# Kernel tuning notes

Hardware: AMD Instinct MI355X
Metric: run time of the kernel (lower is better)

The kernel has to match this reference:

```python
import jax, jax.numpy as jnp
import numpy as np
from jax import lax

NUM_TAGS = 19
IN_DIM = 202
HID = 100
B, T = 256, 512


def setup_inputs() -> dict:
    key = jax.random.key(0)
    ks = jax.random.split(key, 16)
    u = lambda k, shape, s: jax.random.uniform(k, shape, jnp.float32, -s, s)
    sh = 1.0 / np.sqrt(HID)
    sl = 1.0 / np.sqrt(2 * HID)
    x = jax.random.normal(ks[0], (B, T, IN_DIM), jnp.float32)
    lengths = jax.random.randint(ks[1], (B,), 1, T + 1)
    raw_tags = jax.random.randint(ks[2], (B, T), 0, NUM_TAGS)
    y = jnp.where(jnp.arange(T)[None, :] < lengths[:, None], raw_tags, -1)
    return dict(
        x=x, y=y,
        w_ih_f=u(ks[3], (HID, IN_DIM), sh), w_hh_f=u(ks[4], (HID, HID), sh),
        b_ih_f=u(ks[5], (HID,), sh), b_hh_f=u(ks[6], (HID,), sh),
        w_ih_b=u(ks[7], (HID, IN_DIM), sh), w_hh_b=u(ks[8], (HID, HID), sh),
        b_ih_b=u(ks[9], (HID,), sh), b_hh_b=u(ks[10], (HID,), sh),
        w_lin=u(ks[11], (NUM_TAGS, 2 * HID), sl), b_lin=u(ks[12], (NUM_TAGS,), sl),
        start_trans=u(ks[13], (NUM_TAGS,), 0.1),
        end_trans=u(ks[14], (NUM_TAGS,), 0.1),
        trans=u(ks[15], (NUM_TAGS, NUM_TAGS), 0.1),
    )


def _rnn_dir(x, w_ih, w_hh, b_ih, b_hh, reverse):
    # torch nn.RNN (tanh) scans over axis 0 of x (batch_first=False semantics)
    def step(h, xt):
        h = jnp.tanh(xt @ w_ih.T + b_ih + h @ w_hh.T + b_hh)
        return h, h
    h0 = jnp.zeros((x.shape[1], w_hh.shape[0]), x.dtype)
    _, hs = lax.scan(step, h0, x, reverse=reverse)
    return hs  # (S, N, HID)


def _emissions(x, w_ih_f, w_hh_f, b_ih_f, b_hh_f, w_ih_b, w_hh_b, b_ih_b, b_hh_b, w_lin, b_lin):
    hf = _rnn_dir(x, w_ih_f, w_hh_f, b_ih_f, b_hh_f, False)
    hb = _rnn_dir(x, w_ih_b, w_hh_b, b_ih_b, b_hh_b, True)
    h = jnp.concatenate([hf, hb], axis=-1)  # (B, T, 200)
    return jax.nn.softmax(h @ w_lin.T + b_lin, axis=2)  # (B, T, 19)


def _crf_llh(em, tags, mask, start, end, trans):
    # emissions (B,T,K) batch_first -> transpose to (T,B,*) for the scans
    em_t = jnp.swapaxes(em, 0, 1)
    tg = jnp.where(jnp.swapaxes(mask, 0, 1), jnp.swapaxes(tags, 0, 1), 0)
    mk = jnp.swapaxes(mask, 0, 1)
    mf = mk.astype(em.dtype)
    # numerator: gold path score
    s0 = start[tg[0]] + jnp.take_along_axis(em_t[0], tg[0][:, None], 1)[:, 0]
    def num_step(carry, inp):
        s, prev = carry
        e, t, m, mb = inp
        emit = jnp.take_along_axis(e, t[:, None], 1)[:, 0]
        s = s + (trans[prev, t] + emit) * m
        prev = jnp.where(mb, t, prev)  # track tag at last valid position
        return (s, prev), None
    (num, last), _ = lax.scan(num_step, (s0, tg[0]), (em_t[1:], tg[1:], mf[1:], mk[1:]))
    num = num + end[last]
    # denominator: masked forward algorithm
    def z_step(s, inp):
        e, mb = inp
        nxt = jax.nn.logsumexp(s[:, :, None] + trans[None] + e[:, None, :], axis=1)
        return jnp.where(mb[:, None], nxt, s), None
    z, _ = lax.scan(z_step, start + em_t[0], (em_t[1:], mk[1:]))
    logz = jax.nn.logsumexp(z + end, axis=1)
    return num - logz  # (B,) log-likelihood per sequence


def _viterbi(em, mask, start, end, trans):
    em_t = jnp.swapaxes(em, 0, 1)
    mk = jnp.swapaxes(mask, 0, 1)
    def fstep(s, inp):
        e, mb = inp
        cand = s[:, :, None] + trans[None] + e[:, None, :]  # (B,K,K)
        nxt = jnp.where(mb[:, None], jnp.max(cand, axis=1), s)
        return nxt, jnp.argmax(cand, axis=1)
    score, hist = lax.scan(fstep, start + em_t[0], (em_t[1:], mk[1:]))  # hist (T-1,B,K)
    best_last = jnp.argmax(score + end, axis=1)  # tag at each sequence end
    def bstep(tag, inp):
        h, mb = inp
        prev = jnp.take_along_axis(h, tag[:, None], 1)[:, 0]
        tag = jnp.where(mb, prev, tag)
        return tag, tag
    _, tags_bt = lax.scan(bstep, best_last, (hist, mk[1:]), reverse=True)  # (T-1,B), position order
    tags = jnp.concatenate([tags_bt, best_last[None]], axis=0)  # (T,B)
    tags = jnp.swapaxes(tags, 0, 1)
    return jnp.where(mask, tags, -1)  # pad with -1 like the torch pad_sequence


def reference(x, y, w_ih_f, w_hh_f, b_ih_f, b_hh_f, w_ih_b, w_hh_b, b_ih_b, b_hh_b, w_lin, b_lin, start_trans, end_trans, trans):
    mask = y != -1
    em = _emissions(x, w_ih_f, w_hh_f, b_ih_f, b_hh_f, w_ih_b, w_hh_b, b_ih_b, b_hh_b, w_lin, b_lin)
    loss = -jnp.sum(_crf_llh(em, y, mask, start_trans, end_trans, trans))  # reduction='sum'
    label = _viterbi(em, mask, start_trans, end_trans, trans)
    return loss, label
```

## Files before the change

### kernel.cpp

```cpp
#include <hip/hip_runtime.h>
#include <hip/hip_bf16.h>

#define B_ 256
#define T_ 512
#define IN_ 202
#define HID_ 100
#define K_ 19

typedef __attribute__((ext_vector_type(8))) short short8v;
typedef __attribute__((ext_vector_type(4))) float f32x4;

__device__ __forceinline__ float rl_f(float v, int l) {
  return __int_as_float(__builtin_amdgcn_readlane(__float_as_int(v), l));
}
__device__ __forceinline__ float bcast_f(float v, int l) {
  return __int_as_float(__builtin_amdgcn_ds_bpermute(l * 4, __float_as_int(v)));
}
__device__ __forceinline__ float fast_tanh(float x) {
  float t = __expf(2.f * x);
  float r = __builtin_amdgcn_rcpf(t + 1.f);
  return fmaf(-2.f, r, 1.f);
}

__global__ __launch_bounds__(256, 1) void k_wprep(
    const float* __restrict__ wf, const float* __restrict__ wb,
    unsigned short* __restrict__ w3) {
  int idx = blockIdx.x * 256 + threadIdx.x;
  if (idx >= 224 * 224) return;
  int c = idx / 224, k = idx - (idx / 224) * 224;
  float v = 0.f;
  if (k < IN_) {
    if (c < 100) v = wf[c * IN_ + k];
    else if (c < 200) v = wb[(c - 100) * IN_ + k];
  }
  unsigned u0 = __float_as_uint(v) & 0xffff0000u;
  float r1 = v - __uint_as_float(u0);
  unsigned u1 = __float_as_uint(r1) & 0xffff0000u;
  float r2 = r1 - __uint_as_float(u1);
  w3[idx] = (unsigned short)(u0 >> 16);
  w3[50176 + idx] = (unsigned short)(u1 >> 16);
  w3[100352 + idx] = (unsigned short)(__float_as_uint(r2) >> 16);
}

__global__ __launch_bounds__(256, 2) void k_ih(
    const float* __restrict__ x, const unsigned short* __restrict__ w3,
    const float* __restrict__ bif, const float* __restrict__ bhf,
    const float* __restrict__ bib, const float* __restrict__ bhb,
    float* __restrict__ pre) {
  __shared__ float xs[128 * 36];
  __shared__ float bsum[224];
  int tid = threadIdx.x;
  int wv = tid >> 6, l = tid & 63;
  long row0 = (long)blockIdx.x * 128;
  for (int u = tid; u < 224; u += 256) {
    float bv = 0.f;
    if (u < 100) bv = bif[u] + bhf[u];
    else if (u < 200) bv = bib[u - 100] + bhb[u - 100];
    bsum[u] = bv;
  }
  int lr = l & 15;
  int kq = l >> 4;
  f32x4 acc[2][14];
#pragma unroll
  for (int m = 0; m < 2; m++)
#pragma unroll
    for (int n = 0; n < 14; n++) acc[m][n] = (f32x4){0.f, 0.f, 0.f, 0.f};
  for (int ck = 0; ck < 7; ck++) {
    int k0 = ck * 32;
    __syncthreads();
#pragma unroll
    for (int i = 0; i < 8; i++) {
      int u = tid + i * 256;
      int r = u >> 4, kp = u & 15;
      int gk = k0 + 2 * kp;
      float2 v = make_float2(0.f, 0.f);
      if (gk < IN_) v = *(const float2*)(x + (row0 + r) * IN_ + gk);
      *(float2*)(&xs[r * 36 + 2 * kp]) = v;
    }
    __syncthreads();
    short8v A0[2], A1[2], A2[2];
#pragma unroll
    for (int m = 0; m < 2; m++) {
      const float* ap = &xs[(wv * 32 + m * 16 + lr) * 36 + kq * 8];
      float4 fa = *(const float4*)(ap);
      float4 fb = *(const float4*)(ap + 4);
      float f[8] = {fa.x, fa.y, fa.z, fa.w, fb.x, fb.y, fb.z, fb.w};
#pragma unroll
      for (int j = 0; j < 8; j++) {
        unsigned u0 = __float_as_uint(f[j]) & 0xffff0000u;
        float r1 = f[j] - __uint_as_float(u0);
        unsigned u1 = __float_as_uint(r1) & 0xffff0000u;
        float r2 = r1 - __uint_as_float(u1);
        A0[m][j] = (short)(u0 >> 16);
        A1[m][j] = (short)(u1 >> 16);
        A2[m][j] = (short)(__float_as_uint(r2) >> 16);
      }
    }
#pragma unroll
    for (int n = 0; n < 14; n++) {
      int col = n * 16 + lr;
      const unsigned short* bp = w3 + (long)col * 224 + k0 + kq * 8;
      short8v B0 = *(const short8v*)(bp);
      short8v B1 = *(const short8v*)(bp + 50176);
      short8v B2 = *(const short8v*)(bp + 100352);
#pragma unroll
      for (int m = 0; m < 2; m++) {
        f32x4 c = acc[m][n];
        c = __builtin_amdgcn_mfma_f32_16x16x32_bf16(A0[m], B0, c, 0, 0, 0);
        c = __builtin_amdgcn_mfma_f32_16x16x32_bf16(A0[m], B1, c, 0, 0, 0);
        c = __builtin_amdgcn_mfma_f32_16x16x32_bf16(A1[m], B0, c, 0, 0, 0);
        c = __builtin_amdgcn_mfma_f32_16x16x32_bf16(A0[m], B2, c, 0, 0, 0);
        c = __builtin_amdgcn_mfma_f32_16x16x32_bf16(A2[m], B0, c, 0, 0, 0);
        c = __builtin_amdgcn_mfma_f32_16x16x32_bf16(A1[m], B1, c, 0, 0, 0);
        c = __builtin_amdgcn_mfma_f32_16x16x32_bf16(A1[m], B2, c, 0, 0, 0);
        c = __builtin_amdgcn_mfma_f32_16x16x32_bf16(A2[m], B1, c, 0, 0, 0);
        acc[m][n] = c;
      }
    }
  }
#pragma unroll
  for (int m = 0; m < 2; m++) {
    long rbase = row0 + wv * 32 + m * 16 + kq * 4;
#pragma unroll
    for (int n = 0; n < 13; n++) {
      int col = n * 16 + lr;
      if (col < 200) {
        float bv = bsum[col];
#pragma unroll
        for (int r = 0; r < 4; r++)
          pre[(rbase + r) * 200 + col] = acc[m][n][r] + bv;
      }
    }
  }
}

template <int KO, int KN, bool OW>
__device__ __forceinline__ void rnn8(
    float* __restrict__ p, long step, int row, bool owns, int qidx,
    const float* __restrict__ w, float (*hb)[104], float (*ps)[104]) {
  float wr[KN];
#pragma unroll
  for (int i = 0; i < KN / 4; i++) {
    float4 w4 = *(const float4*)(w + row * HID_ + KO + 4 * i);
    wr[4 * i + 0] = w4.x; wr[4 * i + 1] = w4.y;
    wr[4 * i + 2] = w4.z; wr[4 * i + 3] = w4.w;
  }
  float a = 0.f;
  if (OW) a = p[row];
  for (int s = 0; s < B_; s++) {
    int cur = s & 1;
    float a_next = 0.f;
    if (OW && s < B_ - 1) a_next = p[step + row];
    float ac0 = OW ? a : 0.f, ac1 = 0.f, ac2 = 0.f, ac3 = 0.f;
#pragma unroll
    for (int i = 0; i < KN / 4; i++) {
      float4 h4 = *(const float4*)(&hb[cur][KO + 4 * i]);
      ac0 = fmaf(h4.x, wr[4 * i + 0], ac0);
      ac1 = fmaf(h4.y, wr[4 * i + 1], ac1);
      ac2 = fmaf(h4.z, wr[4 * i + 2], ac2);
      ac3 = fmaf(h4.w, wr[4 * i + 3], ac3);
    }
    float partial = (ac0 + ac1) + (ac2 + ac3);
    if (!OW && owns) ps[qidx][row] = partial;
    __syncthreads();
    if (OW) {
      float tot = partial + ps[0][row] + ps[1][row] + ps[2][row];
      float hnew = fast_tanh(tot);
      if (owns) {
        p[row] = hnew;
        hb[cur ^ 1][row] = hnew;
      }
    }
    __syncthreads();
    p += step;
    a = a_next;
  }
}

__global__ __launch_bounds__(512, 8) void k_rnn(
    float* __restrict__ pre,
    const float* __restrict__ whf, const float* __restrict__ whb) {
  __shared__ __align__(16) float hb[2][104];
  __shared__ __align__(16) float ps[3][104];
  int bid = blockIdx.x;
  int dir = bid >> 9;
  int t = bid & 511;
  const float* w = dir ? whb : whf;
  int tid = threadIdx.x;
  int wv = tid >> 6, lane = tid & 63;
  int grp = wv & 1;
  int kq = wv >> 1;
  int row = grp ? (64 + (lane < 36 ? lane : 35)) : lane;
  bool owns = grp ? (lane < 36) : true;
  long step = dir ? -(long)(T_ * 200) : (long)(T_ * 200);
  float* p = pre + ((long)(dir ? (B_ - 1) : 0) * T_ + t) * 200 + dir * 100;
  if (tid < 104) hb[0][tid] = 0.f;
  __syncthreads();
  if (kq == 0)      rnn8<0, 16, true >(p, step, row, owns, 0, w, hb, ps);
  else if (kq == 1) rnn8<16, 28, false>(p, step, row, owns, 0, w, hb, ps);
  else if (kq == 2) rnn8<44, 28, false>(p, step, row, owns, 1, w, hb, ps);
  else              rnn8<72, 28, false>(p, step, row, owns, 2, w, hb, ps);
}

__global__ __launch_bounds__(256, 4) void k_lin(
    const float* __restrict__ h, const float* __restrict__ wlin,
    const float* __restrict__ blin, float* __restrict__ em) {
  int tid = threadIdx.x;
  long r0 = ((long)blockIdx.x * 256 + tid) * 2;
  const float* h0 = h + r0 * 200;
  float acc0[K_], acc1[K_];
#pragma unroll
  for (int c = 0; c < K_; c++) { float bb = blin[c]; acc0[c] = bb; acc1[c] = bb; }
  for (int kk = 0; kk < 50; kk++) {
    float4 a = *(const float4*)(h0 + 4 * kk);
    float4 b = *(const float4*)(h0 + 200 + 4 * kk);
#pragma unroll
    for (int c = 0; c < K_; c++) {
      float4 wv = *(const float4*)(wlin + c * 200 + 4 * kk);
      acc0[c] += a.x * wv.x + a.y * wv.y + a.z * wv.z + a.w * wv.w;
      acc1[c] += b.x * wv.x + b.y * wv.y + b.z * wv.z + b.w * wv.w;
    }
  }
  float mx0 = acc0[0], mx1 = acc1[0];
#pragma unroll
  for (int c = 1; c < K_; c++) { mx0 = fmaxf(mx0, acc0[c]); mx1 = fmaxf(mx1, acc1[c]); }
  float s0 = 0.f, s1 = 0.f;
#pragma unroll
  for (int c = 0; c < K_; c++) {
    acc0[c] = __expf(acc0[c] - mx0); s0 += acc0[c];
    acc1[c] = __expf(acc1[c] - mx1); s1 += acc1[c];
  }
  float i0 = 1.f / s0, i1 = 1.f / s1;
  float* e0 = em + r0 * K_;
#pragma unroll
  for (int c = 0; c < K_; c++) { e0[c] = acc0[c] * i0; e0[K_ + c] = acc1[c] * i1; }
}

__global__ __launch_bounds__(128, 1) void k_crf(
    const float* __restrict__ em, const int* __restrict__ y,
    const float* __restrict__ st_g, const float* __restrict__ en_g,
    const float* __restrict__ tr_g,
    float* __restrict__ part, int* __restrict__ cnt,
    float* __restrict__ out) {
  __shared__ __align__(16) float es[T_ * K_];
  __shared__ int ys[T_];
  __shared__ float trs[K_ * K_];
  __shared__ float st[K_], en[K_];
  __shared__ unsigned char hl[511 * K_ + 13];
  int b = blockIdx.x;
  int tid = threadIdx.x;
  int wv = tid >> 6, lane = tid & 63;
  const float4* eb4 = (const float4*)(em + (long)b * T_ * K_);
  for (int u = tid; u < T_ * K_ / 4; u += 128) ((float4*)es)[u] = eb4[u];
  for (int u = tid; u < T_; u += 128) ys[u] = y[b * T_ + u];
  for (int u = tid; u < K_ * K_; u += 128) trs[u] = tr_g[u];
  if (tid < K_) { st[tid] = st_g[tid]; en[tid] = en_g[tid]; }
  __syncthreads();
  int lmin = T_;
  for (int u = lane; u < T_; u += 64)
    if (ys[u] == -1 && u < lmin) lmin = u;
#pragma unroll
  for (int off = 32; off; off >>= 1) {
    int o = __shfl_xor(lmin, off, 64);
    lmin = lmin < o ? lmin : o;
  }
  int len = lmin;

  int jj = lane < K_ ? lane : K_ - 1;
  bool act = lane < K_;
  float enr[20];
#pragma unroll
  for (int q = 0; q < 5; q++) {
    float4 e4 = (q < 4) ? *(const float4*)(&en[4 * q])
                        : make_float4(en[16], en[17], en[18], -1e30f);
    enr[4 * q] = e4.x; enr[4 * q + 1] = e4.y; enr[4 * q + 2] = e4.z; enr[4 * q + 3] = e4.w;
  }

  if (wv == 0) {
    float gacc = 0.f;
    for (int t = 1 + lane; t < len; t += 64)
      gacc += trs[ys[t - 1] * K_ + ys[t]] + es[t * K_ + ys[t]];
#pragma unroll
    for (int off = 32; off; off >>= 1) gacc += __shfl_xor(gacc, off, 64);
    int y0 = ys[0], ylast = ys[len - 1];
    float num = st[y0] + es[y0] + gacc + en[ylast];
    float Ecol[K_];
#pragma unroll
    for (int i = 0; i < K_; i++) Ecol[i] = __expf(trs[i * K_ + jj]);
    float P = __expf(st[jj] + es[jj]);
    int kacc = 0;
    float ee = __expf(es[K_ + jj]);
    for (int t = 1; t < len; t++) {
      float pr[K_];
#pragma unroll
      for (int i = 0; i < K_; i++) pr[i] = bcast_f(P, i);
      int tn = (t + 1 < T_) ? t + 1 : T_ - 1;
      float e_next = es[tn * K_ + jj];
      unsigned pb = __float_as_uint(pr[0]);
      int ex = (int)((pb >> 23) & 0xff);
      float scale = __uint_as_float((unsigned)(254 - ex) << 23);
      kacc += ex - 127;
      float a0 = 0.f, a1 = 0.f, a2 = 0.f, a3 = 0.f;
#pragma unroll
      for (int i = 0; i < K_; i++) {
        if ((i & 3) == 0)      a0 = fmaf(pr[i], Ecol[i], a0);
        else if ((i & 3) == 1) a1 = fmaf(pr[i], Ecol[i], a1);
        else if ((i & 3) == 2) a2 = fmaf(pr[i], Ecol[i], a2);
        else                   a3 = fmaf(pr[i], Ecol[i], a3);
      }
      P = (((a0 + a1) + (a2 + a3)) * ee) * scale;
      ee = __expf(e_next);
    }
    {
      float pr[K_];
#pragma unroll
      for (int i = 0; i < K_; i++) pr[i] = bcast_f(P, i);
      float sm = 0.f;
#pragma unroll
      for (int i = 0; i < K_; i++) sm += pr[i] * __expf(enr[i]);
      if (lane == 0) part[b] = __logf(sm) + (float)kacc * 0.6931471805599453f - num;
    }
    int old = -1;
    if (lane == 0) { __threadfence(); old = atomicAdd(cnt, 1); }
    old = __shfl(old, 0, 64);
    if (old == B_ - 1) {
      __threadfence();
      float s = 0.f;
      for (int u = lane; u < B_; u += 64) s += part[u];
#pragma unroll
      for (int off = 32; off; off >>= 1) s += __shfl_xor(s, off, 64);
      if (lane == 0) out[0] = s;
    }
  } else {
    float Tt[K_];
#pragma unroll
    for (int i = 0; i < K_; i++) Tt[i] = trs[i * K_ + jj];
    float V = st[jj] + es[jj];
    float e = es[K_ + jj];
    for (int t = 1; t < len; t++) {
      float vr[K_];
#pragma unroll
      for (int i = 0; i < K_; i++) vr[i] = bcast_f(V, i);
      int tn = (t + 1 < T_) ? t + 1 : T_ - 1;
      float e_next = es[tn * K_ + jj];
      float b0 = -1e30f, b1 = -1e30f, b2 = -1e30f, b3 = -1e30f;
      int a0 = 0, a1 = 5, a2 = 10, a3 = 15;
#pragma unroll
      for (int i = 0; i < 5; i++)  { float c = vr[i] + Tt[i]; if (c > b0) { b0 = c; a0 = i; } }
#pragma unroll
      for (int i = 5; i < 10; i++) { float c = vr[i] + Tt[i]; if (c > b1) { b1 = c; a1 = i; } }
#pragma unroll
      for (int i = 10; i < 15; i++){ float c = vr[i] + Tt[i]; if (c > b2) { b2 = c; a2 = i; } }
#pragma unroll
      for (int i = 15; i < 19; i++){ float c = vr[i] + Tt[i]; if (c > b3) { b3 = c; a3 = i; } }
      if (b1 > b0) { b0 = b1; a0 = a1; }
      if (b2 > b0) { b0 = b2; a0 = a2; }
      if (b3 > b0) { b0 = b3; a0 = a3; }
      if (act) hl[(t - 1) * K_ + lane] = (unsigned char)a0;
      V = b0 + e;
      e = e_next;
    }
    int aa;
    {
      float vr[K_];
#pragma unroll
      for (int i = 0; i < K_; i++) vr[i] = bcast_f(V, i);
      float bb = vr[0] + enr[0]; aa = 0;
#pragma unroll
      for (int i = 1; i < K_; i++) {
        float c = vr[i] + enr[i];
        if (c > bb) { bb = c; aa = i; }
      }
    }
    float* ob = out + 1 + (long)b * T_;
    for (int u = lane; u < T_; u += 64)
      if (u >= len) ob[u] = -1.f;
    int tag = aa;
    if (lane == 0) ob[len - 1] = (float)tag;
    int vc = (act && len >= 2) ? (int)hl[(len - 2) * K_ + lane] : 0;
    for (int ti = len - 2; ti >= 0; ti--) {
      int vn = 0;
      if (ti > 0 && act) vn = (int)hl[(ti - 1) * K_ + lane];
      int ts = __builtin_amdgcn_readfirstlane(tag);
      tag = __builtin_amdgcn_readlane(vc, ts);
      if (lane == 0) ob[ti] = (float)tag;
      vc = vn;
    }
  }
}

extern "C" void kernel_launch(void* const* d_in, const int* in_sizes, int n_in,
                              void* d_out, int out_size, void* d_ws, size_t ws_size,
                              hipStream_t stream) {
  const float* x      = (const float*)d_in[0];
  const int*   y      = (const int*)d_in[1];
  const float* w_ih_f = (const float*)d_in[2];
  const float* w_hh_f = (const float*)d_in[3];
  const float* b_ih_f = (const float*)d_in[4];
  const float* b_hh_f = (const float*)d_in[5];
  const float* w_ih_b = (const float*)d_in[6];
  const float* w_hh_b = (const float*)d_in[7];
  const float* b_ih_b = (const float*)d_in[8];
  const float* b_hh_b = (const float*)d_in[9];
  const float* w_lin  = (const float*)d_in[10];
  const float* b_lin  = (const float*)d_in[11];
  const float* st     = (const float*)d_in[12];
  const float* en     = (const float*)d_in[13];
  const float* trans  = (const float*)d_in[14];

  char* ws = (char*)d_ws;
  const size_t PRE_OFF  = 0;
  const size_t EM_OFF   = 104857600;
  const size_t PART_OFF = EM_OFF + 9961472;
  const size_t CNT_OFF  = PART_OFF + 1024;
  float* PRE  = (float*)(ws + PRE_OFF);
  float* EM   = (float*)(ws + EM_OFF);
  float* PART = (float*)(ws + PART_OFF);
  int*   CNT  = (int*)(ws + CNT_OFF);
  unsigned short* W3 = (unsigned short*)(ws + EM_OFF);
  float* out  = (float*)d_out;

  hipMemsetAsync((void*)CNT, 0, sizeof(int), stream);
  k_wprep<<<196, 256, 0, stream>>>(w_ih_f, w_ih_b, W3);
  k_ih<<<1024, 256, 0, stream>>>(x, W3, b_ih_f, b_hh_f, b_ih_b, b_hh_b, PRE);
  k_rnn<<<1024, 512, 0, stream>>>(PRE, w_hh_f, w_hh_b);
  k_lin<<<256, 256, 0, stream>>>(PRE, w_lin, b_lin, EM);
  k_crf<<<256, 128, 0, stream>>>(EM, y, st, en, trans, PART, CNT, out);
}
```

Before: 578.5 us.

## Parallelize CRF forward and Viterbi scans via chunked semiring matrix products

Replaces the serial per-timestep CRF forward-algorithm and Viterbi recurrences with a chunked scan. The 512-step sequence is split into 16-step chunks whose max-plus and sum-product transfer matrices are built in parallel by many wavefronts. Short serial passes then combine the chunk matrices, and Viterbi backpointers are recomputed per chunk from the stored boundary scores. This shortens the serial dependency chain at the cost of far more total arithmetic, 512 threads per block and a large dynamic LDS allocation. The linear-domain chunk products could also lose precision, since rescaling happens only at chunk boundaries.

Measured after the change: 1.431 ms. +147.4%, slower.

```diff
diff --git a/kernel.cpp b/kernel.cpp
--- a/kernel.cpp
+++ b/kernel.cpp
@@ -6,6 +6,25 @@
 #define IN_ 202
 #define HID_ 100
 #define K_ 19
+#define NCH 32
+#define CL 16
+#define MSTRIDE 368
+
+#define MV_OFF   0
+#define MP_OFF   (MV_OFF + NCH * MSTRIDE)
+#define TRT_OFF  (MP_OFF + NCH * MSTRIDE)
+#define ETL_OFF  (TRT_OFF + 380)
+#define BV_OFF   (ETL_OFF + 380)
+#define VF_OFF   (BV_OFF + 640)
+#define PF_OFF   (VF_OFF + 20)
+#define STL_OFF  (PF_OFF + 20)
+#define ENL_OFF  (STL_OFF + 20)
+#define NUM_OFF  (ENL_OFF + 20)
+#define KC_OFF   (NUM_OFF + 2)
+#define FLT_END  (KC_OFF + 2)
+#define HL_OFF_B 100544
+#define LEN_OFF_B (HL_OFF_B + 9728)
+#define CRF_LDS_B (LEN_OFF_B + 64)
 
 typedef __attribute__((ext_vector_type(8))) short short8v;
 typedef __attribute__((ext_vector_type(4))) float f32x4;
@@ -236,147 +255,260 @@
   for (int c = 0; c < K_; c++) { e0[c] = acc0[c] * i0; e0[K_ + c] = acc1[c] * i1; }
 }
 
-__global__ __launch_bounds__(128, 1) void k_crf(
+__global__ __launch_bounds__(512, 1) void k_crf(
     const float* __restrict__ em, const int* __restrict__ y,
     const float* __restrict__ st_g, const float* __restrict__ en_g,
     const float* __restrict__ tr_g,
     float* __restrict__ part, int* __restrict__ cnt,
     float* __restrict__ out) {
-  __shared__ __align__(16) float es[T_ * K_];
-  __shared__ int ys[T_];
-  __shared__ float trs[K_ * K_];
-  __shared__ float st[K_], en[K_];
-  __shared__ unsigned char hl[511 * K_ + 13];
+  extern __shared__ __align__(16) float S[];
+  unsigned char* hl = (unsigned char*)S + HL_OFF_B;
+  int* lenp = (int*)((char*)S + LEN_OFF_B);
   int b = blockIdx.x;
   int tid = threadIdx.x;
   int wv = tid >> 6, lane = tid & 63;
-  const float4* eb4 = (const float4*)(em + (long)b * T_ * K_);
-  for (int u = tid; u < T_ * K_ / 4; u += 128) ((float4*)es)[u] = eb4[u];
-  for (int u = tid; u < T_; u += 128) ys[u] = y[b * T_ + u];
-  for (int u = tid; u < K_ * K_; u += 128) trs[u] = tr_g[u];
-  if (tid < K_) { st[tid] = st_g[tid]; en[tid] = en_g[tid]; }
-  __syncthreads();
-  int lmin = T_;
-  for (int u = lane; u < T_; u += 64)
-    if (ys[u] == -1 && u < lmin) lmin = u;
-#pragma unroll
-  for (int off = 32; off; off >>= 1) {
-    int o = __shfl_xor(lmin, off, 64);
-    lmin = lmin < o ? lmin : o;
-  }
-  int len = lmin;
-
-  int jj = lane < K_ ? lane : K_ - 1;
-  bool act = lane < K_;
-  float enr[20];
-#pragma unroll
-  for (int q = 0; q < 5; q++) {
-    float4 e4 = (q < 4) ? *(const float4*)(&en[4 * q])
-                        : make_float4(en[16], en[17], en[18], -1e30f);
-    enr[4 * q] = e4.x; enr[4 * q + 1] = e4.y; enr[4 * q + 2] = e4.z; enr[4 * q + 3] = e4.w;
-  }
-
+  const float* eb = em + (long)b * T_ * K_;
+  const int* yb = y + (long)b * T_;
+  if (tid < 380) {
+    int j = tid / 20, k = tid - (tid / 20) * 20;
+    float tv = (k < 19) ? tr_g[k * 19 + j] : 0.f;
+    S[TRT_OFF + tid] = tv;
+    S[ETL_OFF + tid] = (k < 19) ? __expf(tv) : 0.f;
+  }
+  if (tid >= 384 && tid < 384 + K_) {
+    int i = tid - 384;
+    S[STL_OFF + i] = st_g[i];
+    S[ENL_OFF + i] = en_g[i];
+  }
+  if (tid == 0) *lenp = T_;
+  __syncthreads();
+  if (yb[tid] == -1) atomicMin(lenp, tid);
+  __syncthreads();
+  int len = *lenp;
+  int nf = (len - 1) >> 4;
+  int rr_ = (len - 1) - (nf << 4);
+
+  int sg = (lane >= 19) + (lane >= 38);
+  bool gact = lane < 57;
+  int li = lane - sg * 19;
+  int gid = wv * 3 + sg;
+
+  for (int rnd = 0; rnd < 2; rnd++) {
+    int c = gid + 24 * rnd;
+    if (gact && c < NCH - 1) {
+      int t0 = CL * c + 1;
+      float m[19], e_[19];
+#pragma unroll
+      for (int j = 0; j < 19; j++) e_[j] = eb[t0 * K_ + j];
+#pragma unroll
+      for (int j = 0; j < 19; j++) m[j] = S[TRT_OFF + j * 20 + li] + e_[j];
+      for (int s = 1; s < CL; s++) {
+        int t = t0 + s;
+#pragma unroll
+        for (int j = 0; j < 19; j++) e_[j] = eb[t * K_ + j];
+        float nm[19];
+#pragma unroll
+        for (int j = 0; j < 19; j++) {
+          const float* tc = &S[TRT_OFF + j * 20];
+          float best = m[0] + tc[0];
+#pragma unroll
+          for (int k = 1; k < 19; k++) best = fmaxf(best, m[k] + tc[k]);
+          nm[j] = best + e_[j];
+        }
+#pragma unroll
+        for (int j = 0; j < 19; j++) m[j] = nm[j];
+      }
+#pragma unroll
+      for (int j = 0; j < 19; j++) S[MV_OFF + c * MSTRIDE + li * 19 + j] = m[j];
+    }
+  }
+  __syncthreads();
+  for (int rnd = 0; rnd < 2; rnd++) {
+    int c = gid + 24 * rnd;
+    if (gact && c < NCH - 1) {
+      int t0 = CL * c + 1;
+      float m[19], ee[19];
+#pragma unroll
+      for (int j = 0; j < 19; j++) ee[j] = __expf(eb[t0 * K_ + j]);
+#pragma unroll
+      for (int j = 0; j < 19; j++) m[j] = S[ETL_OFF + j * 20 + li] * ee[j];
+      for (int s = 1; s < CL; s++) {
+        int t = t0 + s;
+#pragma unroll
+        for (int j = 0; j < 19; j++) ee[j] = __expf(eb[t * K_ + j]);
+        float nm[19];
+#pragma unroll
+        for (int j = 0; j < 19; j++) {
+          const float* ec = &S[ETL_OFF + j * 20];
+          float a0 = 0.f, a1 = 0.f, a2 = 0.f, a3 = 0.f;
+#pragma unroll
+          for (int k = 0; k < 19; k++) {
+            if ((k & 3) == 0)      a0 = fmaf(m[k], ec[k], a0);
+            else if ((k & 3) == 1) a1 = fmaf(m[k], ec[k], a1);
+            else if ((k & 3) == 2) a2 = fmaf(m[k], ec[k], a2);
+            else                   a3 = fmaf(m[k], ec[k], a3);
+          }
+          nm[j] = ((a0 + a1) + (a2 + a3)) * ee[j];
+        }
+#pragma unroll
+        for (int j = 0; j < 19; j++) m[j] = nm[j];
+      }
+#pragma unroll
+      for (int j = 0; j < 19; j++) S[MP_OFF + c * MSTRIDE + li * 19 + j] = m[j];
+    }
+  }
+  __syncthreads();
   if (wv == 0) {
-    float gacc = 0.f;
-    for (int t = 1 + lane; t < len; t += 64)
-      gacc += trs[ys[t - 1] * K_ + ys[t]] + es[t * K_ + ys[t]];
-#pragma unroll
-    for (int off = 32; off; off >>= 1) gacc += __shfl_xor(gacc, off, 64);
-    int y0 = ys[0], ylast = ys[len - 1];
-    float num = st[y0] + es[y0] + gacc + en[ylast];
-    float Ecol[K_];
-#pragma unroll
-    for (int i = 0; i < K_; i++) Ecol[i] = __expf(trs[i * K_ + jj]);
-    float P = __expf(st[jj] + es[jj]);
-    int kacc = 0;
-    float ee = __expf(es[K_ + jj]);
-    for (int t = 1; t < len; t++) {
-      float pr[K_];
-#pragma unroll
-      for (int i = 0; i < K_; i++) pr[i] = bcast_f(P, i);
-      int tn = (t + 1 < T_) ? t + 1 : T_ - 1;
-      float e_next = es[tn * K_ + jj];
+    float Bc = 0.f;
+    if (lane < K_) Bc = S[STL_OFF + lane] + eb[lane];
+    for (int c = 0; c < nf; c++) {
+      if (lane < K_) S[BV_OFF + c * 20 + lane] = Bc;
+      float vr[19];
+#pragma unroll
+      for (int i = 0; i < 19; i++) vr[i] = bcast_f(Bc, i);
+      if (lane < K_) {
+        const float* mc = &S[MV_OFF + c * MSTRIDE];
+        float best = vr[0] + mc[lane];
+#pragma unroll
+        for (int i = 1; i < 19; i++) best = fmaxf(best, vr[i] + mc[i * 19 + lane]);
+        Bc = best;
+      }
+    }
+    if (lane < K_) {
+      S[BV_OFF + nf * 20 + lane] = Bc;
+      if (rr_ == 0) S[VF_OFF + lane] = Bc;
+    }
+  } else if (wv == 1) {
+    float P = 0.f;
+    if (lane < K_) P = __expf(S[STL_OFF + lane] + eb[lane]);
+    int kc = 0;
+    for (int c = 0; c < nf; c++) {
+      float pr[19];
+#pragma unroll
+      for (int i = 0; i < 19; i++) pr[i] = bcast_f(P, i);
       unsigned pb = __float_as_uint(pr[0]);
       int ex = (int)((pb >> 23) & 0xff);
       float scale = __uint_as_float((unsigned)(254 - ex) << 23);
-      kacc += ex - 127;
-      float a0 = 0.f, a1 = 0.f, a2 = 0.f, a3 = 0.f;
-#pragma unroll
-      for (int i = 0; i < K_; i++) {
-        if ((i & 3) == 0)      a0 = fmaf(pr[i], Ecol[i], a0);
-        else if ((i & 3) == 1) a1 = fmaf(pr[i], Ecol[i], a1);
-        else if ((i & 3) == 2) a2 = fmaf(pr[i], Ecol[i], a2);
-        else                   a3 = fmaf(pr[i], Ecol[i], a3);
-      }
-      P = (((a0 + a1) + (a2 + a3)) * ee) * scale;
-      ee = __expf(e_next);
-    }
-    {
-      float pr[K_];
-#pragma unroll
-      for (int i = 0; i < K_; i++) pr[i] = bcast_f(P, i);
-      float sm = 0.f;
-#pragma unroll
-      for (int i = 0; i < K_; i++) sm += pr[i] * __expf(enr[i]);
-      if (lane == 0) part[b] = __logf(sm) + (float)kacc * 0.6931471805599453f - num;
-    }
-    int old = -1;
-    if (lane == 0) { __threadfence(); old = atomicAdd(cnt, 1); }
-    old = __shfl(old, 0, 64);
-    if (old == B_ - 1) {
-      __threadfence();
-      float s = 0.f;
-      for (int u = lane; u < B_; u += 64) s += part[u];
-#pragma unroll
-      for (int off = 32; off; off >>= 1) s += __shfl_xor(s, off, 64);
-      if (lane == 0) out[0] = s;
-    }
-  } else {
-    float Tt[K_];
-#pragma unroll
-    for (int i = 0; i < K_; i++) Tt[i] = trs[i * K_ + jj];
-    float V = st[jj] + es[jj];
-    float e = es[K_ + jj];
-    for (int t = 1; t < len; t++) {
-      float vr[K_];
-#pragma unroll
-      for (int i = 0; i < K_; i++) vr[i] = bcast_f(V, i);
-      int tn = (t + 1 < T_) ? t + 1 : T_ - 1;
-      float e_next = es[tn * K_ + jj];
-      float b0 = -1e30f, b1 = -1e30f, b2 = -1e30f, b3 = -1e30f;
-      int a0 = 0, a1 = 5, a2 = 10, a3 = 15;
-#pragma unroll
-      for (int i = 0; i < 5; i++)  { float c = vr[i] + Tt[i]; if (c > b0) { b0 = c; a0 = i; } }
-#pragma unroll
-      for (int i = 5; i < 10; i++) { float c = vr[i] + Tt[i]; if (c > b1) { b1 = c; a1 = i; } }
-#pragma unroll
-      for (int i = 10; i < 15; i++){ float c = vr[i] + Tt[i]; if (c > b2) { b2 = c; a2 = i; } }
-#pragma unroll
-      for (int i = 15; i < 19; i++){ float c = vr[i] + Tt[i]; if (c > b3) { b3 = c; a3 = i; } }
-      if (b1 > b0) { b0 = b1; a0 = a1; }
-      if (b2 > b0) { b0 = b2; a0 = a2; }
-      if (b3 > b0) { b0 = b3; a0 = a3; }
-      if (act) hl[(t - 1) * K_ + lane] = (unsigned char)a0;
-      V = b0 + e;
-      e = e_next;
-    }
-    int aa;
-    {
-      float vr[K_];
-#pragma unroll
-      for (int i = 0; i < K_; i++) vr[i] = bcast_f(V, i);
-      float bb = vr[0] + enr[0]; aa = 0;
-#pragma unroll
-      for (int i = 1; i < K_; i++) {
-        float c = vr[i] + enr[i];
-        if (c > bb) { bb = c; aa = i; }
-      }
-    }
+      kc += ex - 127;
+#pragma unroll
+      for (int i = 0; i < 19; i++) pr[i] *= scale;
+      if (lane < K_) {
+        const float* mc = &S[MP_OFF + c * MSTRIDE];
+        float a0 = 0.f, a1 = 0.f, a2 = 0.f, a3 = 0.f;
+#pragma unroll
+        for (int i = 0; i < 19; i++) {
+          float mv = mc[i * 19 + lane];
+          if ((i & 3) == 0)      a0 = fmaf(pr[i], mv, a0);
+          else if ((i & 3) == 1) a1 = fmaf(pr[i], mv, a1);
+          else if ((i & 3) == 2) a2 = fmaf(pr[i], mv, a2);
+          else                   a3 = fmaf(pr[i], mv, a3);
+        }
+        P = (a0 + a1) + (a2 + a3);
+      }
+    }
+    for (int s = 0; s < rr_; s++) {
+      int t = (nf << 4) + 1 + s;
+      float pr[19];
+#pragma unroll
+      for (int i = 0; i < 19; i++) pr[i] = bcast_f(P, i);
+      unsigned pb = __float_as_uint(pr[0]);
+      int ex = (int)((pb >> 23) & 0xff);
+      float scale = __uint_as_float((unsigned)(254 - ex) << 23);
+      kc += ex - 127;
+#pragma unroll
+      for (int i = 0; i < 19; i++) pr[i] *= scale;
+      if (lane < K_) {
+        float ee = __expf(eb[t * K_ + lane]);
+        const float* ec = &S[ETL_OFF + lane * 20];
+        float a0 = 0.f, a1 = 0.f, a2 = 0.f, a3 = 0.f;
+#pragma unroll
+        for (int i = 0; i < 19; i++) {
+          if ((i & 3) == 0)      a0 = fmaf(pr[i], ec[i], a0);
+          else if ((i & 3) == 1) a1 = fmaf(pr[i], ec[i], a1);
+          else if ((i & 3) == 2) a2 = fmaf(pr[i], ec[i], a2);
+          else                   a3 = fmaf(pr[i], ec[i], a3);
+        }
+        P = ((a0 + a1) + (a2 + a3)) * ee;
+      }
+    }
+    if (lane < K_) S[PF_OFF + lane] = P;
+    if (lane == 0) *(int*)&S[KC_OFF] = kc;
+  } else if (wv == 2) {
+    float gacc = 0.f;
+    for (int t = 1 + lane; t < len; t += 64) {
+      int yp = yb[t - 1], yc = yb[t];
+      gacc += S[TRT_OFF + yc * 20 + yp] + eb[t * K_ + yc];
+    }
+#pragma unroll
+    for (int off = 32; off; off >>= 1) gacc += __shfl_xor(gacc, off, 64);
+    if (lane == 0) {
+      int y0 = yb[0], yl = yb[len - 1];
+      S[NUM_OFF] = S[STL_OFF + y0] + eb[y0] + gacc + S[ENL_OFF + yl];
+    }
+  } else if (wv == 3) {
     float* ob = out + 1 + (long)b * T_;
     for (int u = lane; u < T_; u += 64)
       if (u >= len) ob[u] = -1.f;
+  }
+  __syncthreads();
+  if (wv == 0) {
+    int c = lane;
+    if (c <= nf && c < NCH) {
+      int nst = (c < nf) ? CL : rr_;
+      if (nst > 0) {
+        float v[19];
+#pragma unroll
+        for (int k = 0; k < 19; k++) v[k] = S[BV_OFF + c * 20 + k];
+        for (int s = 0; s < nst; s++) {
+          int t = (c << 4) + 1 + s;
+          float e_[19];
+#pragma unroll
+          for (int j = 0; j < 19; j++) e_[j] = eb[t * K_ + j];
+          float nv[19];
+#pragma unroll
+          for (int j = 0; j < 19; j++) {
+            const float* tc = &S[TRT_OFF + j * 20];
+            float best = v[0] + tc[0];
+            int bi = 0;
+#pragma unroll
+            for (int k = 1; k < 19; k++) {
+              float cd = v[k] + tc[k];
+              if (cd > best) { best = cd; bi = k; }
+            }
+            hl[(t - 1) * K_ + j] = (unsigned char)bi;
+            nv[j] = best + e_[j];
+          }
+#pragma unroll
+          for (int j = 0; j < 19; j++) v[j] = nv[j];
+        }
+        if (c == nf) {
+#pragma unroll
+          for (int k = 0; k < 19; k++) S[VF_OFF + k] = v[k];
+        }
+      }
+    }
+  } else if (wv == 1) {
+    if (lane == 0) {
+      int kc = *(int*)&S[KC_OFF];
+      float sm = 0.f;
+#pragma unroll
+      for (int i = 0; i < 19; i++) sm += S[PF_OFF + i] * __expf(S[ENL_OFF + i]);
+      part[b] = __logf(sm) + (float)kc * 0.6931471805599453f - S[NUM_OFF];
+    }
+  }
+  __syncthreads();
+  if (wv == 0) {
+    float bb = S[VF_OFF + 0] + S[ENL_OFF + 0];
+    int aa = 0;
+#pragma unroll
+    for (int i = 1; i < 19; i++) {
+      float cd = S[VF_OFF + i] + S[ENL_OFF + i];
+      if (cd > bb) { bb = cd; aa = i; }
+    }
+    float* ob = out + 1 + (long)b * T_;
     int tag = aa;
     if (lane == 0) ob[len - 1] = (float)tag;
+    bool act = lane < K_;
     int vc = (act && len >= 2) ? (int)hl[(len - 2) * K_ + lane] : 0;
     for (int ti = len - 2; ti >= 0; ti--) {
       int vn = 0;
@@ -385,6 +517,18 @@
       tag = __builtin_amdgcn_readlane(vc, ts);
       if (lane == 0) ob[ti] = (float)tag;
       vc = vn;
+    }
+  } else if (wv == 1) {
+    int old = -1;
+    if (lane == 0) { __threadfence(); old = atomicAdd(cnt, 1); }
+    old = __shfl(old, 0, 64);
+    if (old == B_ - 1) {
+      __threadfence();
+      float s = 0.f;
+      for (int u = lane; u < B_; u += 64) s += part[u];
+#pragma unroll
+      for (int off = 32; off; off >>= 1) s += __shfl_xor(s, off, 64);
+      if (lane == 0) out[0] = s;
     }
   }
 }
@@ -420,10 +564,12 @@
   unsigned short* W3 = (unsigned short*)(ws + EM_OFF);
   float* out  = (float*)d_out;
 
+  hipFuncSetAttribute((const void*)k_crf,
+                      hipFuncAttributeMaxDynamicSharedMemorySize, CRF_LDS_B);
   hipMemsetAsync((void*)CNT, 0, sizeof(int), stream);
   k_wprep<<<196, 256, 0, stream>>>(w_ih_f, w_ih_b, W3);
   k_ih<<<1024, 256, 0, stream>>>(x, W3, b_ih_f, b_hh_f, b_ih_b, b_hh_b, PRE);
   k_rnn<<<1024, 512, 0, stream>>>(PRE, w_hh_f, w_hh_b);
   k_lin<<<256, 256, 0, stream>>>(PRE, w_lin, b_lin, EM);
-  k_crf<<<256, 128, 0, stream>>>(EM, y, st, en, trans, PART, CNT, out);
-}
+  k_crf<<<256, 512, CRF_LDS_B, stream>>>(EM, y, st, en, trans, PART, CNT, out);
+}
```
